# Kernel optimization log

Hardware: AMD Instinct MI355X
Metric: run time of the kernel (lower is better)

## Reference

```python
import jax, jax.numpy as jnp
import numpy as np

N_NODES = 50000
N_EDGES = 1600000
HIDDEN = 512
LN_EPS = 1e-5


def setup_inputs() -> dict:
    key = jax.random.key(0)
    k1, k2, k3, k4 = jax.random.split(key, 4)
    label_emb = jax.random.normal(k1, (N_NODES, HIDDEN), dtype=jnp.float32)
    edge_index = jax.random.randint(k2, (2, N_EDGES), 0, N_NODES, dtype=jnp.int64)
    W = jax.random.normal(k3, (HIDDEN, HIDDEN), dtype=jnp.float32) / np.sqrt(HIDDEN)
    b = jnp.zeros((HIDDEN,), dtype=jnp.float32)
    gamma = jnp.ones((HIDDEN,), dtype=jnp.float32)
    beta = jnp.zeros((HIDDEN,), dtype=jnp.float32)
    return {"label_emb": label_emb, "edge_index": edge_index, "W": W, "b": b,
            "gamma": gamma, "beta": beta}


def _gcn_conv(x, src, dst, W, b, n_nodes):
    loops = jnp.arange(n_nodes, dtype=src.dtype)
    src_all = jnp.concatenate([src, loops])  # [E+N]
    dst_all = jnp.concatenate([dst, loops])
    ones = jnp.ones_like(dst_all, dtype=x.dtype)
    deg = jax.ops.segment_sum(ones, dst_all, num_segments=n_nodes)  # [N]
    dinv = jnp.where(deg > 0, jax.lax.rsqrt(deg), 0.0)
    norm = dinv[src_all] * dinv[dst_all]  # [E+N]
    h = x @ W  # [N, H] dense transform first (fewer FLOPs than per-edge)
    msgs = h[src_all] * norm[:, None]  # gather + per-edge scale
    out = jax.ops.segment_sum(msgs, dst_all, num_segments=n_nodes)  # scatter-add
    return out + b


def reference(label_emb, edge_index, W, b, gamma, beta):
    residual = label_emb
    src, dst = edge_index[0], edge_index[1]
    h = _gcn_conv(label_emb, src, dst, W, b, N_NODES)
    # dropout is identity at inference (training=False)
    h = residual + h
    mean = jnp.mean(h, axis=-1, keepdims=True)
    var = jnp.var(h, axis=-1, keepdims=True)
    h = (h - mean) * jax.lax.rsqrt(var + LN_EPS) * gamma + beta
    return h
```

## Files before the change

kernel.cpp:

```cpp
#include <hip/hip_runtime.h>

#define HID 512
#define CAP 128
#define BINCAP 384

typedef unsigned int uint32;
using bf16x8 = __attribute__((ext_vector_type(8))) short;
using f32x4  = __attribute__((ext_vector_type(4))) float;
using f32x2  = __attribute__((ext_vector_type(2))) float;
using u32x2  = __attribute__((ext_vector_type(2))) unsigned int;
using u32x4  = __attribute__((ext_vector_type(4))) unsigned int;
using u16x4  = __attribute__((ext_vector_type(4))) unsigned short;
using u16x8  = __attribute__((ext_vector_type(8))) unsigned short;

__device__ __forceinline__ unsigned short f2bf(float f) {
    uint32 u = __float_as_uint(f);
    uint32 r = (u + 0x7FFFu + ((u >> 16) & 1u)) >> 16;
    return (unsigned short)r;
}
__device__ __forceinline__ float bf2f(unsigned short u) {
    return __uint_as_float(((uint32)u) << 16);
}

__device__ __forceinline__ void gl_lds16(const unsigned short* g, unsigned short* l) {
    __builtin_amdgcn_global_load_lds(
        (const __attribute__((address_space(1))) void*)g,
        (__attribute__((address_space(3))) void*)l,
        16, 0, 0);
}

__global__ __launch_bounds__(256) void prep_bin(const int* __restrict__ src,
                                                const int* __restrict__ dst,
                                                int* __restrict__ bincnt,
                                                uint32* __restrict__ bins, int e,
                                                const float* __restrict__ X,
                                                unsigned short* __restrict__ Xbf,
                                                const float* __restrict__ W,
                                                unsigned short* __restrict__ Wt,
                                                int n_elems, int pad_elems,
                                                int nbb, int nbx) {
    const int bid = blockIdx.x;
    if (bid < nbb) {
        for (int i = bid * 256 + (int)threadIdx.x; i < e; i += nbb * 256) {
            int d = dst[i], s = src[i];
            int b = d >> 3;
            int p = atomicAdd(&bincnt[b], 1);
            bins[(size_t)b * BINCAP + p] = ((uint32)(d & 7) << 16) | (uint32)s;
        }
    } else if (bid < nbb + nbx) {
        int base = ((bid - nbb) * 256 + threadIdx.x) * 8;
        if (base < n_elems) {
            f32x4 a = *(const f32x4*)(X + base);
            f32x4 b = *(const f32x4*)(X + base + 4);
            u16x4 w0, w1;
            w0[0] = f2bf(a[0]); w0[1] = f2bf(a[1]); w0[2] = f2bf(a[2]); w0[3] = f2bf(a[3]);
            w1[0] = f2bf(b[0]); w1[1] = f2bf(b[1]); w1[2] = f2bf(b[2]); w1[3] = f2bf(b[3]);
            *(u16x4*)(Xbf + base) = w0;
            *(u16x4*)(Xbf + base + 4) = w1;
        } else if (base < pad_elems) {
            u16x4 z = {0, 0, 0, 0};
            *(u16x4*)(Xbf + base) = z;
            *(u16x4*)(Xbf + base + 4) = z;
        }
    } else {
        int idx = (bid - nbb - nbx) * 256 + threadIdx.x;
        if (idx < HID * HID) {
            int k = idx >> 9, n = idx & (HID - 1);
            Wt[n * HID + k] = f2bf(W[k * HID + n]);
        }
    }
}

#define NWGX 4
__global__ __launch_bounds__(256) void csr_gemm(const uint32* __restrict__ bins,
                                                const int* __restrict__ bincnt,
                                                unsigned short* __restrict__ csrf,
                                                int* __restrict__ fill,
                                                float* __restrict__ dinvf,
                                                const unsigned short* __restrict__ Xbf,
                                                const unsigned short* __restrict__ Wt,
                                                unsigned char* __restrict__ hs8,
                                                int nslices, int nwg) {
    __shared__ alignas(16) unsigned char smem[128 * CAP * 2 + 128 * 4];

    if ((int)blockIdx.x < nslices) {
        unsigned short* lcs = (unsigned short*)smem;
        int* lcnt = (int*)(smem + 128 * CAP * 2);
        const int b = blockIdx.x;
        for (int j = threadIdx.x; j < 128; j += 256) lcnt[j] = 0;
        __syncthreads();
        #pragma unroll
        for (int sb = 0; sb < 16; ++sb) {
            const int gb = b * 16 + sb;
            const int m = bincnt[gb];
            const uint32* be = bins + (size_t)gb * BINCAP;
            for (int i = threadIdx.x; i < m; i += 256) {
                uint32 ev = be[i];
                int ln = sb * 8 + (int)(ev >> 16);
                int p = atomicAdd(&lcnt[ln], 1);
                lcs[ln * CAP + p] = (unsigned short)(ev & 0xFFFFu);
            }
        }
        __syncthreads();
        u32x4* gout = (u32x4*)(csrf + (size_t)b * 128 * CAP);
        const u32x4* lin = (const u32x4*)lcs;
        for (int j = threadIdx.x; j < 128 * CAP / 8; j += 256) gout[j] = lin[j];
        if (threadIdx.x < 128) {
            int c = lcnt[threadIdx.x];
            fill[b * 128 + threadIdx.x] = c;
            dinvf[b * 128 + threadIdx.x] = rsqrtf((float)c + 1.0f);
        }
        return;
    }

    unsigned short* Alds = (unsigned short*)smem;
    unsigned short* Blds = (unsigned short*)(smem + 128 * 64 * 2);
    const int bx = (int)blockIdx.x - nslices;
    const int cpx = nwg >> 3;
    const int swz = (bx & 7) * cpx + (bx >> 3);
    const int row_base = (swz >> 2) * 128;
    const int col_base = (swz & 3) * 128;

    const int t = threadIdx.x;
    const int lane = t & 63, wid = t >> 6;
    const int wm = wid >> 1, wn = wid & 1;

    const int srow = lane >> 3;
    const int gch  = ((lane & 7) ^ srow) * 8;
    const unsigned short* gA = Xbf + (size_t)(row_base + wid * 8 + srow) * HID + gch;
    const unsigned short* gB = Wt  + (size_t)(col_base + wid * 8 + srow) * HID + gch;
    unsigned short* lA = &Alds[wid * 512];
    unsigned short* lB = &Blds[wid * 512];

    f32x4 acc[4][4];
    #pragma unroll
    for (int m = 0; m < 4; ++m)
        #pragma unroll
        for (int n = 0; n < 4; ++n)
            acc[m][n] = (f32x4){0.f, 0.f, 0.f, 0.f};

    const int rr = lane & 15;
    const int kg8 = lane >> 4;

    for (int k0 = 0; k0 < HID; k0 += 64) {
        #pragma unroll
        for (int rd = 0; rd < 4; ++rd) {
            gl_lds16(gA + (size_t)rd * 32 * HID + k0, lA + rd * 2048);
            gl_lds16(gB + (size_t)rd * 32 * HID + k0, lB + rd * 2048);
        }
        __syncthreads();

        bf16x8 afr[4][2], bfr[4][2];
        #pragma unroll
        for (int m = 0; m < 4; ++m) {
            int row = wm * 64 + m * 16 + rr;
            #pragma unroll
            for (int ks = 0; ks < 2; ++ks)
                afr[m][ks] = *(const bf16x8*)&Alds[row * 64 + (((ks * 4 + kg8) ^ (row & 7)) * 8)];
        }
        #pragma unroll
        for (int n = 0; n < 4; ++n) {
            int row = wn * 64 + n * 16 + rr;
            #pragma unroll
            for (int ks = 0; ks < 2; ++ks)
                bfr[n][ks] = *(const bf16x8*)&Blds[row * 64 + (((ks * 4 + kg8) ^ (row & 7)) * 8)];
        }
        #pragma unroll
        for (int ks = 0; ks < 2; ++ks)
            #pragma unroll
            for (int m = 0; m < 4; ++m)
                #pragma unroll
                for (int n = 0; n < 4; ++n)
                    acc[m][n] = __builtin_amdgcn_mfma_f32_16x16x32_bf16(afr[m][ks], bfr[n][ks], acc[m][n], 0, 0, 0);
        __syncthreads();
    }

    const int rgrp = (lane >> 4) * 4;
    const int cc = lane & 15;
    #pragma unroll
    for (int m = 0; m < 4; ++m) {
        #pragma unroll
        for (int r = 0; r < 4; ++r) {
            int grow = row_base + wm * 64 + m * 16 + rgrp + r;
            #pragma unroll
            for (int n = 0; n < 4; ++n) {
                int gcol = col_base + wn * 64 + n * 16 + cc;
                float v = acc[m][n][r];
                unsigned int p = __builtin_amdgcn_cvt_pk_fp8_f32(v, v, 0u, false);
                hs8[(size_t)grow * HID + gcol] = (unsigned char)p;
            }
        }
    }
}

__device__ __forceinline__ void dec8s(u32x2 v, float g, float* acc) {
    f32x2 a = __builtin_amdgcn_cvt_pk_f32_fp8(v[0], false);
    f32x2 b = __builtin_amdgcn_cvt_pk_f32_fp8(v[0], true);
    f32x2 c = __builtin_amdgcn_cvt_pk_f32_fp8(v[1], false);
    f32x2 d = __builtin_amdgcn_cvt_pk_f32_fp8(v[1], true);
    acc[0] += g * a[0]; acc[1] += g * a[1]; acc[2] += g * b[0]; acc[3] += g * b[1];
    acc[4] += g * c[0]; acc[5] += g * c[1]; acc[6] += g * d[0]; acc[7] += g * d[1];
}

__global__ __launch_bounds__(256) void agg_ln(const unsigned char* __restrict__ hs8,
                                              const float* __restrict__ resid,
                                              const float* __restrict__ bvec,
                                              const float* __restrict__ gamma,
                                              const float* __restrict__ beta,
                                              const int* __restrict__ fill,
                                              const float* __restrict__ dinvf,
                                              const unsigned short* __restrict__ csrf,
                                              float* __restrict__ out, int nn) {
    const int wave = threadIdx.x >> 6;
    const int lane = threadIdx.x & 63;
    const int n = blockIdx.x * 4 + wave;
    if (n >= nn) return;
    const int c0 = lane * 8;

    const float gn = dinvf[n];
    float acc[8];
    #pragma unroll
    for (int j = 0; j < 8; ++j) acc[j] = 0.f;
    dec8s(*(const u32x2*)(hs8 + (size_t)n * HID + c0), gn, acc);

    const int m = fill[n];
    const unsigned short* idx = csrf + (size_t)n * CAP;
    int i = 0;
    for (; i + 8 <= m; i += 8) {
        u16x8 iv = *(const u16x8*)(idx + i);
        float g0 = dinvf[iv[0]], g1 = dinvf[iv[1]], g2 = dinvf[iv[2]], g3 = dinvf[iv[3]];
        float g4 = dinvf[iv[4]], g5 = dinvf[iv[5]], g6 = dinvf[iv[6]], g7 = dinvf[iv[7]];
        u32x2 v0 = *(const u32x2*)(hs8 + (size_t)iv[0] * HID + c0);
        u32x2 v1 = *(const u32x2*)(hs8 + (size_t)iv[1] * HID + c0);
        u32x2 v2 = *(const u32x2*)(hs8 + (size_t)iv[2] * HID + c0);
        u32x2 v3 = *(const u32x2*)(hs8 + (size_t)iv[3] * HID + c0);
        u32x2 v4 = *(const u32x2*)(hs8 + (size_t)iv[4] * HID + c0);
        u32x2 v5 = *(const u32x2*)(hs8 + (size_t)iv[5] * HID + c0);
        u32x2 v6 = *(const u32x2*)(hs8 + (size_t)iv[6] * HID + c0);
        u32x2 v7 = *(const u32x2*)(hs8 + (size_t)iv[7] * HID + c0);
        dec8s(v0, g0, acc); dec8s(v1, g1, acc); dec8s(v2, g2, acc); dec8s(v3, g3, acc);
        dec8s(v4, g4, acc); dec8s(v5, g5, acc); dec8s(v6, g6, acc); dec8s(v7, g7, acc);
    }
    for (; i < m; ++i) {
        int s = idx[i];
        dec8s(*(const u32x2*)(hs8 + (size_t)s * HID + c0), dinvf[s], acc);
    }

    f32x4 r0 = __builtin_nontemporal_load((const f32x4*)(resid + (size_t)n * HID + c0));
    f32x4 r1 = __builtin_nontemporal_load((const f32x4*)(resid + (size_t)n * HID + c0 + 4));
    float val[8];
    #pragma unroll
    for (int j = 0; j < 4; ++j) {
        val[j]     = r0[j] + gn * acc[j]     + bvec[c0 + j];
        val[j + 4] = r1[j] + gn * acc[j + 4] + bvec[c0 + j + 4];
    }

    float s = 0.f, q = 0.f;
    #pragma unroll
    for (int j = 0; j < 8; ++j) { s += val[j]; q += val[j] * val[j]; }
    #pragma unroll
    for (int off = 32; off > 0; off >>= 1) {
        s += __shfl_xor(s, off, 64);
        q += __shfl_xor(q, off, 64);
    }
    const float mean = s * (1.f / 512.f);
    const float var = q * (1.f / 512.f) - mean * mean;
    const float rstd = rsqrtf(var + 1e-5f);

    f32x4 o0, o1;
    #pragma unroll
    for (int j = 0; j < 4; ++j) {
        o0[j] = (val[j]     - mean) * rstd * gamma[c0 + j]     + beta[c0 + j];
        o1[j] = (val[j + 4] - mean) * rstd * gamma[c0 + j + 4] + beta[c0 + j + 4];
    }
    __builtin_nontemporal_store(o0, (f32x4*)(out + (size_t)n * HID + c0));
    __builtin_nontemporal_store(o1, (f32x4*)(out + (size_t)n * HID + c0 + 4));
}

extern "C" void kernel_launch(void* const* d_in, const int* in_sizes, int n_in,
                              void* d_out, int out_size, void* d_ws, size_t ws_size,
                              hipStream_t stream) {
    const float* X     = (const float*)d_in[0];
    const int*   edges = (const int*)d_in[1];
    const float* W     = (const float*)d_in[2];
    const float* b     = (const float*)d_in[3];
    const float* gamma = (const float*)d_in[4];
    const float* beta  = (const float*)d_in[5];
    float* out = (float*)d_out;

    const int E = in_sizes[1] / 2;
    const int N = in_sizes[0] / HID;
    const int M_pad = ((N + 255) / 256) * 256;
    const int nslices = M_pad / 128;
    const int nbins = M_pad / 8;
    const int* src = edges;
    const int* dst = edges + E;

    char* w = (char*)d_ws;
    auto alloc = [&](size_t bytes) { char* p = w; w += (bytes + 255) & ~(size_t)255; return p; };
    int*    fill   = (int*)alloc((size_t)M_pad * 4);
    float*  dinvf  = (float*)alloc((size_t)M_pad * 4);
    int*    bincnt = (int*)alloc((size_t)nbins * 4);
    uint32* bins   = (uint32*)alloc((size_t)nbins * BINCAP * 4);
    unsigned short* csrf = (unsigned short*)alloc((size_t)M_pad * CAP * 2);
    unsigned short* Wt   = (unsigned short*)alloc((size_t)HID * HID * 2);
    unsigned char*  hs8  = (unsigned char*)alloc((size_t)M_pad * HID);
    unsigned short* Xbf = (unsigned short*)d_out;

    hipMemsetAsync(bincnt, 0, (size_t)nbins * 4, stream);

    const int pad_elems = M_pad * HID;
    const int nbb = 2048;
    const int nbx = (pad_elems / 8 + 255) / 256;
    const int nbw = (HID * HID + 255) / 256;
    prep_bin<<<nbb + nbx + nbw, 256, 0, stream>>>(src, dst, bincnt, bins, E,
                                                  X, Xbf, W, Wt,
                                                  N * HID, pad_elems, nbb, nbx);

    const int nwg = (M_pad / 128) * NWGX;
    csr_gemm<<<nslices + nwg, 256, 0, stream>>>(bins, bincnt, csrf, fill, dinvf,
                                                Xbf, Wt, hs8, nslices, nwg);

    agg_ln<<<(N + 3) / 4, 256, 0, stream>>>(hs8, X, b, gamma, beta, fill, dinvf, csrf, out, N);
}
```

Baseline: 277.1 us.

## Fuse fp32-to-bf16 conversion of X into GEMM A-tile loads

Removes the separate pass that converts the node features to a padded bf16 buffer. The GEMM now streams fp32 X tiles straight into LDS, clamping out-of-range rows, and packs them to bf16 in registers before the MFMAs. This avoids writing and re-reading a bf16 copy of X. In exchange it doubles LDS footprint and global load bytes for the A operand, and adds conversion work inside the GEMM inner loop, which each of the 4 column tiles repeats.

```diff
diff --git a/kernel.cpp b/kernel.cpp
--- a/kernel.cpp
+++ b/kernel.cpp
@@ -1,4 +1,5 @@
 #include <hip/hip_runtime.h>
+#include <hip/hip_bf16.h>
 
 #define HID 512
 #define CAP 128
@@ -18,27 +19,33 @@
     uint32 r = (u + 0x7FFFu + ((u >> 16) & 1u)) >> 16;
     return (unsigned short)r;
 }
-__device__ __forceinline__ float bf2f(unsigned short u) {
-    return __uint_as_float(((uint32)u) << 16);
-}
-
-__device__ __forceinline__ void gl_lds16(const unsigned short* g, unsigned short* l) {
+
+__device__ __forceinline__ void gl_lds16(const void* g, void* l) {
     __builtin_amdgcn_global_load_lds(
         (const __attribute__((address_space(1))) void*)g,
         (__attribute__((address_space(3))) void*)l,
         16, 0, 0);
 }
 
+__device__ __forceinline__ bf16x8 pack_bf16x8(f32x4 lo, f32x4 hi) {
+    union { bf16x8 v; unsigned short u[8]; } r;
+    #pragma unroll
+    for (int z = 0; z < 4; ++z) {
+        union { __hip_bfloat16 h; unsigned short u; } a, b;
+        a.h = __float2bfloat16(lo[z]);
+        b.h = __float2bfloat16(hi[z]);
+        r.u[z] = a.u; r.u[z + 4] = b.u;
+    }
+    return r.v;
+}
+
 __global__ __launch_bounds__(256) void prep_bin(const int* __restrict__ src,
                                                 const int* __restrict__ dst,
                                                 int* __restrict__ bincnt,
                                                 uint32* __restrict__ bins, int e,
-                                                const float* __restrict__ X,
-                                                unsigned short* __restrict__ Xbf,
                                                 const float* __restrict__ W,
                                                 unsigned short* __restrict__ Wt,
-                                                int n_elems, int pad_elems,
-                                                int nbb, int nbx) {
+                                                int nbb) {
     const int bid = blockIdx.x;
     if (bid < nbb) {
         for (int i = bid * 256 + (int)threadIdx.x; i < e; i += nbb * 256) {
@@ -47,23 +54,8 @@
             int p = atomicAdd(&bincnt[b], 1);
             bins[(size_t)b * BINCAP + p] = ((uint32)(d & 7) << 16) | (uint32)s;
         }
-    } else if (bid < nbb + nbx) {
-        int base = ((bid - nbb) * 256 + threadIdx.x) * 8;
-        if (base < n_elems) {
-            f32x4 a = *(const f32x4*)(X + base);
-            f32x4 b = *(const f32x4*)(X + base + 4);
-            u16x4 w0, w1;
-            w0[0] = f2bf(a[0]); w0[1] = f2bf(a[1]); w0[2] = f2bf(a[2]); w0[3] = f2bf(a[3]);
-            w1[0] = f2bf(b[0]); w1[1] = f2bf(b[1]); w1[2] = f2bf(b[2]); w1[3] = f2bf(b[3]);
-            *(u16x4*)(Xbf + base) = w0;
-            *(u16x4*)(Xbf + base + 4) = w1;
-        } else if (base < pad_elems) {
-            u16x4 z = {0, 0, 0, 0};
-            *(u16x4*)(Xbf + base) = z;
-            *(u16x4*)(Xbf + base + 4) = z;
-        }
     } else {
-        int idx = (bid - nbb - nbx) * 256 + threadIdx.x;
+        int idx = (bid - nbb) * 256 + threadIdx.x;
         if (idx < HID * HID) {
             int k = idx >> 9, n = idx & (HID - 1);
             Wt[n * HID + k] = f2bf(W[k * HID + n]);
@@ -77,11 +69,11 @@
                                                 unsigned short* __restrict__ csrf,
                                                 int* __restrict__ fill,
                                                 float* __restrict__ dinvf,
-                                                const unsigned short* __restrict__ Xbf,
+                                                const float* __restrict__ Xf,
                                                 const unsigned short* __restrict__ Wt,
                                                 unsigned char* __restrict__ hs8,
-                                                int nslices, int nwg) {
-    __shared__ alignas(16) unsigned char smem[128 * CAP * 2 + 128 * 4];
+                                                int nslices, int nwg, int nreal) {
+    __shared__ alignas(16) unsigned char smem[49152];
 
     if ((int)blockIdx.x < nslices) {
         unsigned short* lcs = (unsigned short*)smem;
@@ -113,8 +105,8 @@
         return;
     }
 
-    unsigned short* Alds = (unsigned short*)smem;
-    unsigned short* Blds = (unsigned short*)(smem + 128 * 64 * 2);
+    float* Aldsf = (float*)smem;
+    unsigned short* Blds = (unsigned short*)(smem + 32768);
     const int bx = (int)blockIdx.x - nslices;
     const int cpx = nwg >> 3;
     const int swz = (bx & 7) * cpx + (bx >> 3);
@@ -125,11 +117,12 @@
     const int lane = t & 63, wid = t >> 6;
     const int wm = wid >> 1, wn = wid & 1;
 
+    const int arow4 = lane >> 4;
+    const int ach   = (lane & 15) >> 1;
+    const int ahalf = lane & 1;
     const int srow = lane >> 3;
     const int gch  = ((lane & 7) ^ srow) * 8;
-    const unsigned short* gA = Xbf + (size_t)(row_base + wid * 8 + srow) * HID + gch;
-    const unsigned short* gB = Wt  + (size_t)(col_base + wid * 8 + srow) * HID + gch;
-    unsigned short* lA = &Alds[wid * 512];
+    const unsigned short* gB = Wt + (size_t)(col_base + wid * 8 + srow) * HID + gch;
     unsigned short* lB = &Blds[wid * 512];
 
     f32x4 acc[4][4];
@@ -144,10 +137,17 @@
 
     for (int k0 = 0; k0 < HID; k0 += 64) {
         #pragma unroll
-        for (int rd = 0; rd < 4; ++rd) {
-            gl_lds16(gA + (size_t)rd * 32 * HID + k0, lA + rd * 2048);
+        for (int rd = 0; rd < 8; ++rd) {
+            int r = wid * 32 + rd * 4 + arow4;
+            int grow = row_base + r;
+            if (grow >= nreal) grow = nreal - 1;
+            int sw = ((ach ^ (r & 7)) << 3) + ahalf * 4;
+            gl_lds16(Xf + (size_t)grow * HID + k0 + sw,
+                     Aldsf + (size_t)(wid * 32 + rd * 4) * 64);
+        }
+        #pragma unroll
+        for (int rd = 0; rd < 4; ++rd)
             gl_lds16(gB + (size_t)rd * 32 * HID + k0, lB + rd * 2048);
-        }
         __syncthreads();
 
         bf16x8 afr[4][2], bfr[4][2];
@@ -155,8 +155,13 @@
         for (int m = 0; m < 4; ++m) {
             int row = wm * 64 + m * 16 + rr;
             #pragma unroll
-            for (int ks = 0; ks < 2; ++ks)
-                afr[m][ks] = *(const bf16x8*)&Alds[row * 64 + (((ks * 4 + kg8) ^ (row & 7)) * 8)];
+            for (int ks = 0; ks < 2; ++ks) {
+                int off = (((ks * 4 + kg8) ^ (row & 7)) << 3);
+                const float* ap = &Aldsf[(size_t)(row << 6) + off];
+                f32x4 lo = *(const f32x4*)ap;
+                f32x4 hi = *(const f32x4*)(ap + 4);
+                afr[m][ks] = pack_bf16x8(lo, hi);
+            }
         }
         #pragma unroll
         for (int n = 0; n < 4; ++n) {
@@ -305,21 +310,16 @@
     unsigned short* csrf = (unsigned short*)alloc((size_t)M_pad * CAP * 2);
     unsigned short* Wt   = (unsigned short*)alloc((size_t)HID * HID * 2);
     unsigned char*  hs8  = (unsigned char*)alloc((size_t)M_pad * HID);
-    unsigned short* Xbf = (unsigned short*)d_out;
 
     hipMemsetAsync(bincnt, 0, (size_t)nbins * 4, stream);
 
-    const int pad_elems = M_pad * HID;
     const int nbb = 2048;
-    const int nbx = (pad_elems / 8 + 255) / 256;
     const int nbw = (HID * HID + 255) / 256;
-    prep_bin<<<nbb + nbx + nbw, 256, 0, stream>>>(src, dst, bincnt, bins, E,
-                                                  X, Xbf, W, Wt,
-                                                  N * HID, pad_elems, nbb, nbx);
+    prep_bin<<<nbb + nbw, 256, 0, stream>>>(src, dst, bincnt, bins, E, W, Wt, nbb);
 
     const int nwg = (M_pad / 128) * NWGX;
     csr_gemm<<<nslices + nwg, 256, 0, stream>>>(bins, bincnt, csrf, fill, dinvf,
-                                                Xbf, Wt, hs8, nslices, nwg);
+                                                X, Wt, hs8, nslices, nwg, N);
 
     agg_ln<<<(N + 3) / 4, 256, 0, stream>>>(hs8, X, b, gamma, beta, fill, dinvf, csrf, out, N);
 }
```

Result: no change. 272.3 us (-1.7%).
